# Kernel optimization log

Measured on AMD Instinct MI355X. Metric: run time of the kernel, lower is better.

The kernel has to match this reference:

```python
import jax, jax.numpy as jnp
import numpy as np

DIM = 2048
NHEADS = 32
HEAD_DIM = DIM // NHEADS
EPS = 1e-6


def _rmsnorm(t):
    # RMSNorm over last dim, no weight
    return t * jax.lax.rsqrt(jnp.mean(t * t, axis=-1, keepdims=True) + EPS)


def setup_inputs() -> dict:
    key = jax.random.key(0)
    kx, kc, kq, kk, kv = jax.random.split(key, 5)
    x = jax.random.normal(kx, (2, 4096, DIM), dtype=jnp.float32)
    context = jax.random.normal(kc, (2, 512, DIM), dtype=jnp.float32)
    std = 0.02
    Wq = jax.random.normal(kq, (DIM, DIM), dtype=jnp.float32) * std
    Wk = jax.random.normal(kk, (DIM, DIM), dtype=jnp.float32) * std
    Wv = jax.random.normal(kv, (DIM, DIM), dtype=jnp.float32) * std
    return {"x": x, "context": context, "Wq": Wq, "Wk": Wk, "Wv": Wv}


def reference(x, context, Wq, Wk, Wv):
    b, n, _ = x.shape
    m = context.shape[1]
    # projections (torch Linear: y = x @ W.T, no bias)
    q = x @ Wq.T                      # (b, n, dim)
    k_raw = context @ Wk.T            # (b, m, dim)
    v_raw = context @ Wv.T            # (b, m, dim)

    # split q into heads: b n (h d) -> b h n d
    q = q.reshape(b, n, NHEADS, HEAD_DIM).transpose(0, 2, 1, 3)

    # faithful to the original: cat(k,v) then 'b n (h d j)' with j=2
    kv = jnp.concatenate([k_raw, v_raw], axis=-1)          # (b, m, 2*dim)
    kv = kv.reshape(b, m, NHEADS, HEAD_DIM, 2)             # (h d j) factorization
    k = kv[..., 0].transpose(0, 2, 1, 3)                   # (b, h, m, d)
    v = kv[..., 1].transpose(0, 2, 1, 3)                   # (b, h, m, d)

    # per-head QK RMSNorm (no weight)
    q = _rmsnorm(q)
    k = _rmsnorm(k)

    scale = HEAD_DIM ** -0.5
    scores = jnp.einsum('bhnd,bhmd->bhnm', q, k) * scale
    attn = jax.nn.softmax(scores, axis=-1)
    out = jnp.einsum('bhnm,bhmd->bhnd', attn, v)           # (b, h, n, d)
    # back to (b, n, dim)
    return out.transpose(0, 2, 1, 3).reshape(b, n, NHEADS * HEAD_DIM)
```

## Files before the change

### kernel.cpp

```cpp
#include <hip/hip_runtime.h>
#include <cstdint>


typedef unsigned short u16;
typedef unsigned int u32;
typedef __bf16 bf16x8 __attribute__((ext_vector_type(8)));
typedef float f32x4 __attribute__((ext_vector_type(4)));
typedef float f32x16 __attribute__((ext_vector_type(16)));

__device__ __forceinline__ u16 f2bf(float f) {
  union { float f; unsigned u; } a; a.f = f;
  unsigned r = a.u + 0x7FFFu + ((a.u >> 16) & 1u);
  return (u16)(r >> 16);
}

__device__ __forceinline__ void gload_lds16(const u16* g, u16* l) {
  __builtin_amdgcn_global_load_lds((const __attribute__((address_space(1))) void*)g,
                                   (__attribute__((address_space(3))) void*)l, 16, 0, 0);
}

__global__ __launch_bounds__(256) void cvt_bf16(const float4* __restrict__ in,
                                                uint2* __restrict__ out, int n4) {
  int i = blockIdx.x * 256 + threadIdx.x;
  if (i >= n4) return;
  float4 v = in[i];
  uint2 o;
  o.x = (unsigned)f2bf(v.x) | ((unsigned)f2bf(v.y) << 16);
  o.y = (unsigned)f2bf(v.z) | ((unsigned)f2bf(v.w) << 16);
  out[i] = o;
}

__global__ __launch_bounds__(512, 2) void qgemm256(const u16* __restrict__ A,
                                                   const u16* __restrict__ B,
                                                   u16* __restrict__ QN) {
  constexpr int K = 2048, T = 32;
  __shared__ __align__(16) u16 As[2][256 * 64];
  __shared__ __align__(16) u16 Bs[2][256 * 64];
  const int t = threadIdx.x;
  const int wid = t >> 6, l = t & 63;
  const int wr = wid >> 2, wc = wid & 3;
  const int lr = l & 15, lg = l >> 4;
  const int bid = blockIdx.x;
  const int bx = bid >> 3, by = bid & 7;
  const int brow = bx << 8, bcol = by << 8;

  const int srcu = ((l & 7) ^ (l >> 3)) << 3;
  const int growA = brow + (wid << 3) + (l >> 3);
  const int growB = bcol + (wid << 3) + (l >> 3);

  const int u2k0 = ((lg ^ (l & 7)) << 3);
  const int u2k1 = u2k0 ^ 32;
  const int rbA = (((wr << 7) + lr) << 6);
  const int rbB = (((wc << 6) + lr) << 6);

  f32x4 acc[8][4] = {};

  auto stage = [&](int buf, int half, int kto, bool isB) {
    const u16* gp = isB ? B : A;
    const int grow = (isB ? growB : growA) + (half << 7);
    u16* lb = (isB ? Bs[buf] : As[buf]) + (half << 13) + (wid << 9);
#pragma unroll
    for (int i = 0; i < 2; ++i)
      gload_lds16(gp + (size_t)(grow + (i << 6)) * K + kto + srcu, lb + (i << 12));
  };

  stage(0, 0, 0, false); stage(0, 1, 0, false);
  stage(0, 0, 0, true);  stage(0, 1, 0, true);
  asm volatile("s_waitcnt vmcnt(0)" ::: "memory");
  __builtin_amdgcn_s_barrier();

  for (int tt = 0; tt < T; ++tt) {
    const int bufc = tt & 1, bufn = bufc ^ 1;
    const int kto = (tt + 1) << 6;
    const bool pre = (tt + 1 < T);

    if (pre) {
      stage(bufn, 0, kto, false); stage(bufn, 1, kto, false);
      stage(bufn, 0, kto, true);  stage(bufn, 1, kto, true);
      asm volatile("s_waitcnt vmcnt(8)" ::: "memory");
    } else {
      asm volatile("s_waitcnt vmcnt(0)" ::: "memory");
    }
    __builtin_amdgcn_sched_barrier(0);
    __builtin_amdgcn_s_barrier();
    __builtin_amdgcn_sched_barrier(0);

    bf16x8 bfr[4][2];
#pragma unroll
    for (int ni = 0; ni < 4; ++ni) {
      bfr[ni][0] = *(const bf16x8*)&Bs[bufc][rbB + (ni << 10) + u2k0];
      bfr[ni][1] = *(const bf16x8*)&Bs[bufc][rbB + (ni << 10) + u2k1];
    }
#pragma unroll
    for (int g = 0; g < 4; ++g) {
      bf16x8 af[2][2];
#pragma unroll
      for (int j = 0; j < 2; ++j) {
        af[j][0] = *(const bf16x8*)&As[bufc][rbA + (((g << 1) + j) << 10) + u2k0];
        af[j][1] = *(const bf16x8*)&As[bufc][rbA + (((g << 1) + j) << 10) + u2k1];
      }
#pragma unroll
      for (int j = 0; j < 2; ++j)
#pragma unroll
        for (int ni = 0; ni < 4; ++ni)
#pragma unroll
          for (int kk = 0; kk < 2; ++kk)
            acc[(g << 1) + j][ni] = __builtin_amdgcn_mfma_f32_16x16x32_bf16(
                af[j][kk], bfr[ni][kk], acc[(g << 1) + j][ni], 0, 0, 0);
    }

    __builtin_amdgcn_sched_barrier(0);
    __builtin_amdgcn_s_barrier();
  }

  const int head = (by << 2) + wc;
#pragma unroll
  for (int mi = 0; mi < 8; ++mi) {
#pragma unroll
    for (int r = 0; r < 4; ++r) {
      float ss = 0.f;
#pragma unroll
      for (int ni = 0; ni < 4; ++ni) { float v = acc[mi][ni][r]; ss += v * v; }
      ss += __shfl_xor(ss, 1); ss += __shfl_xor(ss, 2);
      ss += __shfl_xor(ss, 4); ss += __shfl_xor(ss, 8);
      const float sc = rsqrtf(ss * (1.f / 64.f) + 1e-6f) * (0.125f * 1.4426950408889634f);
      const int row = brow + (wr << 7) + (mi << 4) + (lg << 2) + r;
      const int b = row >> 12, n = row & 4095;
      u16* o = QN + ((size_t)((b << 5) + head) * 4096 + n) * 64;
#pragma unroll
      for (int ni = 0; ni < 4; ++ni)
        o[(ni << 4) + lr] = f2bf(acc[mi][ni][r] * sc);
    }
  }
}

__global__ __launch_bounds__(256) void gemm_bt(const u16* __restrict__ A,
                                               const u16* __restrict__ B,
                                               float* __restrict__ C, int ldc) {
  constexpr int K = 2048;
  __shared__ __align__(16) u16 As[128 * 32];
  __shared__ __align__(16) u16 Bs[128 * 32];
  const int t = threadIdx.x;
  const int w = t >> 6, l = t & 63;
  const int wr = w >> 1, wc = w & 1;
  const int lr = l & 15, lg = l >> 4;
  const int brow = blockIdx.x << 7, bcol = blockIdx.y << 7;

  f32x4 acc[4][4] = {};

  const int c0 = (w << 6) + l;
  const u16* Ab = A + (size_t)brow * K;
  const u16* Bb = B + (size_t)bcol * K;

  for (int kt = 0; kt < K; kt += 32) {
    __syncthreads();
#pragma unroll
    for (int i = 0; i < 2; ++i) {
      const int c = (i << 8) + c0;
      const int row = c >> 2, koff = (c & 3) << 3;
      gload_lds16(Ab + (size_t)row * K + kt + koff, As + (((i << 8) + (w << 6)) << 3));
      gload_lds16(Bb + (size_t)row * K + kt + koff, Bs + (((i << 8) + (w << 6)) << 3));
    }
    __syncthreads();
    bf16x8 af[4], bfr[4];
#pragma unroll
    for (int mi = 0; mi < 4; ++mi)
      af[mi] = *(const bf16x8*)&As[(((wr << 6) + (mi << 4) + lr) << 5) + (lg << 3)];
#pragma unroll
    for (int ni = 0; ni < 4; ++ni)
      bfr[ni] = *(const bf16x8*)&Bs[(((wc << 6) + (ni << 4) + lr) << 5) + (lg << 3)];
#pragma unroll
    for (int mi = 0; mi < 4; ++mi)
#pragma unroll
      for (int ni = 0; ni < 4; ++ni)
        acc[mi][ni] = __builtin_amdgcn_mfma_f32_16x16x32_bf16(af[mi], bfr[ni], acc[mi][ni], 0, 0, 0);
  }

#pragma unroll
  for (int mi = 0; mi < 4; ++mi)
#pragma unroll
    for (int r = 0; r < 4; ++r) {
      const int row = brow + (wr << 6) + (mi << 4) + (lg << 2) + r;
      float* o = C + (size_t)row * ldc + bcol + (wc << 6);
#pragma unroll
      for (int ni = 0; ni < 4; ++ni)
        o[(ni << 4) + lr] = acc[mi][ni][r];
    }
}

__global__ __launch_bounds__(256) void kvbuild2(const float* __restrict__ kv,
                                                u16* __restrict__ kn,
                                                u16* __restrict__ vtn) {
  __shared__ u16 Vl[64][72];
  const int t = threadIdx.x;
  const int bh = blockIdx.x >> 3, mt = blockIdx.x & 7;
  const int b = bh >> 5, h = bh & 31;
  const int mloc = t >> 2, dc = (t & 3) << 4;
  const int m = (mt << 6) + mloc;
  const float2* src = (const float2*)(kv + ((size_t)((b << 9) + m)) * 4096 + ((h >> 4) << 11))
                      + ((h & 15) << 6) + dc;
  float kvals[16], vvals[16];
  float ss = 0.f;
#pragma unroll
  for (int dd = 0; dd < 16; ++dd) {
    float2 p = src[dd];
    kvals[dd] = p.x; vvals[dd] = p.y;
    ss += p.x * p.x;
  }
  ss += __shfl_xor(ss, 1); ss += __shfl_xor(ss, 2);
  const float sc = rsqrtf(ss * (1.f / 64.f) + 1e-6f);
  union { uint4 u4[2]; u16 h[16]; } ko;
#pragma unroll
  for (int dd = 0; dd < 16; ++dd) ko.h[dd] = f2bf(kvals[dd] * sc);
  u16* kdst = kn + ((size_t)bh * 512 + m) * 64 + dc;
  *(uint4*)kdst = ko.u4[0];
  *(uint4*)(kdst + 8) = ko.u4[1];
#pragma unroll
  for (int dd = 0; dd < 16; ++dd) Vl[dc + dd][mloc] = f2bf(vvals[dd]);
  __syncthreads();
  const int drow = t >> 2, mc = (t & 3) << 4;
  uint4 r0 = *(const uint4*)&Vl[drow][mc];
  uint4 r1 = *(const uint4*)&Vl[drow][mc + 8];
  u16* vdst = vtn + ((size_t)(bh << 6) + drow) * 512 + (mt << 6) + mc;
  *(uint4*)vdst = r0;
  *(uint4*)(vdst + 8) = r1;
}

__global__ __launch_bounds__(256) void attn4(const u16* __restrict__ qn,
                                             const u16* __restrict__ kn,
                                             const u16* __restrict__ vtn,
                                             float* __restrict__ out) {
  __shared__ __align__(16) u16 Kt[64 * 68];
  __shared__ __align__(16) u16 Vt[64 * 68];
  const int t = threadIdx.x, w = t >> 6, l = t & 63;
  const int i31 = l & 31, hi = l >> 5;
  const int nblk = blockIdx.x, bh = blockIdx.y;
  const int b = bh >> 5, h = bh & 31;
  const int qrow = (nblk << 7) + (w << 5) + i31;

  const u16* qb = qn + ((size_t)bh * 4096 + qrow) * 64 + (hi << 3);
  bf16x8 bq[4];
#pragma unroll
  for (int kt = 0; kt < 4; ++kt) bq[kt] = *(const bf16x8*)(qb + (kt << 4));

  f32x16 po[2];
#pragma unroll
  for (int d = 0; d < 2; ++d)
#pragma unroll
    for (int r = 0; r < 16; ++r) po[d][r] = 0.f;
  float lrun = 0.f;

  const u16* kb = kn + ((size_t)bh << 9) * 64;
  const u16* vb = vtn + ((size_t)bh << 6) * 512;
  const int srow = t >> 2, sp = (t & 3) << 3;

  for (int mt = 0; mt < 8; ++mt) {
    __syncthreads();
    {
      const u16* gk = kb + (size_t)((mt << 6) + srow) * 64 + sp;
      uint4 a0 = *(const uint4*)gk;
      uint4 a1 = *(const uint4*)(gk + 32);
      const u16* gv = vb + (size_t)srow * 512 + (mt << 6) + sp;
      uint4 b0 = *(const uint4*)gv;
      uint4 b1 = *(const uint4*)(gv + 32);
      *(uint4*)&Kt[srow * 68 + sp] = a0;
      *(uint4*)&Kt[srow * 68 + sp + 32] = a1;
      *(uint4*)&Vt[srow * 68 + sp] = b0;
      *(uint4*)&Vt[srow * 68 + sp + 32] = b1;
    }
    __syncthreads();

    f32x16 fs[2];
    __builtin_amdgcn_s_setprio(1);
#pragma unroll
    for (int jt = 0; jt < 2; ++jt) {
      f32x16 s = {};
#pragma unroll
      for (int kt = 0; kt < 4; ++kt) {
        const bf16x8 ak = *(const bf16x8*)&Kt[((jt << 5) + i31) * 68 + (kt << 4) + (hi << 3)];
        s = __builtin_amdgcn_mfma_f32_32x32x16_bf16(ak, bq[kt], s, 0, 0, 0);
      }
      fs[jt] = s;
    }
    __builtin_amdgcn_s_setprio(0);

    float rs = 0.f;
    u32 pq[2][4][2];
#pragma unroll
    for (int jt = 0; jt < 2; ++jt)
#pragma unroll
      for (int q = 0; q < 4; ++q)
#pragma unroll
        for (int rp = 0; rp < 2; ++rp) {
          const float p0 = exp2f(fs[jt][(q << 2) + (rp << 1)]);
          const float p1 = exp2f(fs[jt][(q << 2) + (rp << 1) + 1]);
          rs += p0 + p1;
          union { u32 u; __bf16 h2[2]; } pk;
          pk.h2[0] = (__bf16)p0;
          pk.h2[1] = (__bf16)p1;
          pq[jt][q][rp] = pk.u;
        }
    rs += __shfl_xor(rs, 32);
    lrun += rs;

    __builtin_amdgcn_s_setprio(1);
#pragma unroll
    for (int kk = 0; kk < 4; ++kk) {
      const int jt = kk >> 1, q0 = (kk & 1) << 1;
      union { u32 wd[4]; bf16x8 v; } pf;
#pragma unroll
      for (int rp = 0; rp < 2; ++rp) {
        const u32 v0 = pq[jt][q0][rp], v1 = pq[jt][q0 + 1][rp];
        const u32 send = hi ? v0 : v1;
        const u32 ex = (u32)__shfl_xor((int)send, 32);
        pf.wd[rp] = hi ? ex : v0;
        pf.wd[2 + rp] = hi ? v1 : ex;
      }
#pragma unroll
      for (int dt = 0; dt < 2; ++dt) {
        const bf16x8 av = *(const bf16x8*)&Vt[((dt << 5) + i31) * 68 + (kk << 4) + (hi << 3)];
        po[dt] = __builtin_amdgcn_mfma_f32_32x32x16_bf16(av, pf.v, po[dt], 0, 0, 0);
      }
    }
    __builtin_amdgcn_s_setprio(0);
  }

  const float inv = 1.f / lrun;
  float* ob = out + ((size_t)(b << 12) + qrow) * 2048 + (h << 6) + (hi << 2);
#pragma unroll
  for (int dt = 0; dt < 2; ++dt)
#pragma unroll
    for (int q = 0; q < 4; ++q) {
      float4 v = { po[dt][(q << 2)] * inv, po[dt][(q << 2) + 1] * inv,
                   po[dt][(q << 2) + 2] * inv, po[dt][(q << 2) + 3] * inv };
      *(float4*)(ob + (dt << 5) + (q << 3)) = v;
    }
}

extern "C" void kernel_launch(void* const* d_in, const int* in_sizes, int n_in,
                              void* d_out, int out_size, void* d_ws, size_t ws_size,
                              hipStream_t stream) {
  const float* x   = (const float*)d_in[0];
  const float* ctx = (const float*)d_in[1];
  const float* Wq  = (const float*)d_in[2];
  const float* Wk  = (const float*)d_in[3];
  const float* Wv  = (const float*)d_in[4];
  float* out = (float*)d_out;
  char* ws = (char*)d_ws;

  u16* xb   = (u16*)(ws + 0);
  u16* cb   = (u16*)(ws + 33554432);
  u16* Wqb  = (u16*)(ws + 37748736);
  u16* Wkb  = (u16*)(ws + 46137344);
  u16* Wvb  = (u16*)(ws + 54525952);
  u16* qnp  = (u16*)(ws + 62914560);
  float* kvraw = (float*)(ws + 0);
  u16* knp  = (u16*)(ws + 16777216);
  u16* vtnp = (u16*)(ws + 20971520);

  cvt_bf16<<<16384, 256, 0, stream>>>((const float4*)x,   (uint2*)xb,  4194304);
  cvt_bf16<<<2048,  256, 0, stream>>>((const float4*)ctx, (uint2*)cb,   524288);
  cvt_bf16<<<4096,  256, 0, stream>>>((const float4*)Wq,  (uint2*)Wqb, 1048576);
  cvt_bf16<<<4096,  256, 0, stream>>>((const float4*)Wk,  (uint2*)Wkb, 1048576);
  cvt_bf16<<<4096,  256, 0, stream>>>((const float4*)Wv,  (uint2*)Wvb, 1048576);

  qgemm256<<<256, 512, 0, stream>>>(xb, Wqb, qnp);
  gemm_bt<<<dim3(8, 32), 256, 0, stream>>>(cb, Wkb, kvraw, 4096);
  kvbuild2<<<512, 256, 0, stream>>>(kvraw, knp, vtnp);
  attn4<<<dim3(32, 64), 256, 0, stream>>>(qnp, knp, vtnp, out);
}
```

Measured before the change: 359.9 us.

## Merge bf16 conversions into one launch and software-pipeline LDS reads with MFMA

Replaces five separate fp32-to-bf16 conversion launches with a single kernel that selects the source by index range and writes into a contiguous workspace, removing per-launch overhead. In the Q GEMM inner loop, A-fragment LDS reads are double-buffered so that reads for the next quad are issued before the MFMAs of the current quad, separated by sched_barriers, and the MFMA blocks are raised in priority with s_setprio. This aims to hide LDS latency behind matrix instructions, at the cost of more live registers under a 2-waves-per-SIMD launch bound.

New measurement: 346.6 us. 1.04x faster.

```diff
diff --git a/kernel.cpp b/kernel.cpp
--- a/kernel.cpp
+++ b/kernel.cpp
@@ -19,16 +19,45 @@
                                    (__attribute__((address_space(3))) void*)l, 16, 0, 0);
 }
 
-__global__ __launch_bounds__(256) void cvt_bf16(const float4* __restrict__ in,
-                                                uint2* __restrict__ out, int n4) {
-  int i = blockIdx.x * 256 + threadIdx.x;
-  if (i >= n4) return;
-  float4 v = in[i];
+__global__ __launch_bounds__(256) void cvt_all(const float4* __restrict__ x,
+                                               const float4* __restrict__ ctx,
+                                               const float4* __restrict__ wq,
+                                               const float4* __restrict__ wk,
+                                               const float4* __restrict__ wv,
+                                               uint2* __restrict__ dst) {
+  const int i = blockIdx.x * 256 + threadIdx.x;
+  const float4* s;
+  int off;
+  if (i < 4194304)      { s = x;   off = 0; }
+  else if (i < 4718592) { s = ctx; off = 4194304; }
+  else if (i < 5767168) { s = wq;  off = 4718592; }
+  else if (i < 6815744) { s = wk;  off = 5767168; }
+  else                  { s = wv;  off = 6815744; }
+  float4 v = s[i - off];
   uint2 o;
   o.x = (unsigned)f2bf(v.x) | ((unsigned)f2bf(v.y) << 16);
   o.y = (unsigned)f2bf(v.z) | ((unsigned)f2bf(v.w) << 16);
-  out[i] = o;
-}
+  dst[i] = o;
+}
+
+#define READ_QUAD(dst, mi0)                                                    \
+  _Pragma("unroll")                                                            \
+  for (int j = 0; j < 2; ++j) {                                                \
+    dst[j][0] = *(const bf16x8*)&As[bufc][rbA + (((mi0) + j) << 10) + u2k0];   \
+    dst[j][1] = *(const bf16x8*)&As[bufc][rbA + (((mi0) + j) << 10) + u2k1];   \
+  }
+
+#define MFMA_QUAD(src, mi0)                                                    \
+  __builtin_amdgcn_s_setprio(1);                                               \
+  _Pragma("unroll")                                                            \
+  for (int j = 0; j < 2; ++j)                                                  \
+    _Pragma("unroll")                                                          \
+    for (int ni = 0; ni < 4; ++ni)                                             \
+      _Pragma("unroll")                                                        \
+      for (int kk = 0; kk < 2; ++kk)                                           \
+        acc[(mi0) + j][ni] = __builtin_amdgcn_mfma_f32_16x16x32_bf16(          \
+            src[j][kk], bfr[ni][kk], acc[(mi0) + j][ni], 0, 0, 0);             \
+  __builtin_amdgcn_s_setprio(0);
 
 __global__ __launch_bounds__(512, 2) void qgemm256(const u16* __restrict__ A,
                                                    const u16* __restrict__ B,
@@ -91,23 +120,22 @@
       bfr[ni][0] = *(const bf16x8*)&Bs[bufc][rbB + (ni << 10) + u2k0];
       bfr[ni][1] = *(const bf16x8*)&Bs[bufc][rbB + (ni << 10) + u2k1];
     }
-#pragma unroll
-    for (int g = 0; g < 4; ++g) {
-      bf16x8 af[2][2];
-#pragma unroll
-      for (int j = 0; j < 2; ++j) {
-        af[j][0] = *(const bf16x8*)&As[bufc][rbA + (((g << 1) + j) << 10) + u2k0];
-        af[j][1] = *(const bf16x8*)&As[bufc][rbA + (((g << 1) + j) << 10) + u2k1];
-      }
-#pragma unroll
-      for (int j = 0; j < 2; ++j)
-#pragma unroll
-        for (int ni = 0; ni < 4; ++ni)
-#pragma unroll
-          for (int kk = 0; kk < 2; ++kk)
-            acc[(g << 1) + j][ni] = __builtin_amdgcn_mfma_f32_16x16x32_bf16(
-                af[j][kk], bfr[ni][kk], acc[(g << 1) + j][ni], 0, 0, 0);
-    }
+    bf16x8 afA[2][2], afB[2][2];
+    READ_QUAD(afA, 0)
+    __builtin_amdgcn_sched_barrier(0);
+    READ_QUAD(afB, 2)
+    __builtin_amdgcn_sched_barrier(0);
+    MFMA_QUAD(afA, 0)
+    __builtin_amdgcn_sched_barrier(0);
+    READ_QUAD(afA, 4)
+    __builtin_amdgcn_sched_barrier(0);
+    MFMA_QUAD(afB, 2)
+    __builtin_amdgcn_sched_barrier(0);
+    READ_QUAD(afB, 6)
+    __builtin_amdgcn_sched_barrier(0);
+    MFMA_QUAD(afA, 4)
+    __builtin_amdgcn_sched_barrier(0);
+    MFMA_QUAD(afB, 6)
 
     __builtin_amdgcn_sched_barrier(0);
     __builtin_amdgcn_s_barrier();
@@ -352,17 +380,14 @@
   u16* cb   = (u16*)(ws + 33554432);
   u16* Wqb  = (u16*)(ws + 37748736);
   u16* Wkb  = (u16*)(ws + 46137344);
-  u16* Wvb  = (u16*)(ws + 54525952);
   u16* qnp  = (u16*)(ws + 62914560);
   float* kvraw = (float*)(ws + 0);
   u16* knp  = (u16*)(ws + 16777216);
   u16* vtnp = (u16*)(ws + 20971520);
 
-  cvt_bf16<<<16384, 256, 0, stream>>>((const float4*)x,   (uint2*)xb,  4194304);
-  cvt_bf16<<<2048,  256, 0, stream>>>((const float4*)ctx, (uint2*)cb,   524288);
-  cvt_bf16<<<4096,  256, 0, stream>>>((const float4*)Wq,  (uint2*)Wqb, 1048576);
-  cvt_bf16<<<4096,  256, 0, stream>>>((const float4*)Wk,  (uint2*)Wkb, 1048576);
-  cvt_bf16<<<4096,  256, 0, stream>>>((const float4*)Wv,  (uint2*)Wvb, 1048576);
+  cvt_all<<<30720, 256, 0, stream>>>((const float4*)x, (const float4*)ctx,
+                                     (const float4*)Wq, (const float4*)Wk,
+                                     (const float4*)Wv, (uint2*)ws);
 
   qgemm256<<<256, 512, 0, stream>>>(xb, Wqb, qnp);
   gemm_bt<<<dim3(8, 32), 256, 0, stream>>>(cb, Wkb, kvraw, 4096);
```
